# Kernel tuning notes

Hardware: AMD Instinct MI355X
Metric: run time of the kernel (lower is better)

Reference implementation:

```python
import jax, jax.numpy as jnp
import numpy as np

N_QUBITS = 12
DEPTH = 6
BATCH = 4096

# Wire 0 is the most-significant bit (PennyLane default.qubit convention).

def _rx(t):
    c = jnp.cos(t / 2).astype(jnp.complex64)
    s = (-1j * jnp.sin(t / 2)).astype(jnp.complex64)
    return jnp.stack([jnp.stack([c, s], -1), jnp.stack([s, c], -1)], -2)

def _ry(t):
    c = jnp.cos(t / 2).astype(jnp.complex64)
    s = jnp.sin(t / 2).astype(jnp.complex64)
    return jnp.stack([jnp.stack([c, -s], -1), jnp.stack([s, c], -1)], -2)

def _rz(t):
    em = jnp.exp(-1j * t.astype(jnp.complex64) / 2)
    ep = jnp.exp(1j * t.astype(jnp.complex64) / 2)
    z = jnp.zeros_like(em)
    return jnp.stack([jnp.stack([em, z], -1), jnp.stack([z, ep], -1)], -2)

def _apply_1q(state, gate, q, n):
    # state: (B, 2^n); gate: (2,2) shared or (B,2,2) batched
    B = state.shape[0]
    st = state.reshape(B, 1 << q, 2, 1 << (n - 1 - q))
    eq = 'ab,xlbr->xlar' if gate.ndim == 2 else 'xab,xlbr->xlar'
    return jnp.einsum(eq, gate, st).reshape(B, -1)

def _apply_cnot(state, c, n):
    # CNOT with control c, target c+1 (adjacent wires)
    B = state.shape[0]
    st = state.reshape(B, 1 << c, 2, 2, 1 << (n - 2 - c))
    st = jnp.concatenate([st[:, :, 0:1], st[:, :, 1:2, ::-1]], axis=2)
    return st.reshape(B, -1)

def _z_signs(n):
    idx = jnp.arange(1 << n)
    bits = (idx[None, :] >> (n - 1 - jnp.arange(n))[:, None]) & 1  # (n, 2^n)
    return (1.0 - 2.0 * bits).astype(jnp.float32)

def setup_inputs() -> dict:
    key = jax.random.key(0)
    k1, k2 = jax.random.split(key)
    x = jax.random.normal(k1, (BATCH, N_QUBITS), dtype=jnp.float32)
    params = jax.random.normal(k2, (DEPTH, N_QUBITS, 3), dtype=jnp.float32)
    return {"x": x, "params": params}

def reference(x, params):
    B, n = x.shape
    depth = params.shape[0]
    state = jnp.zeros((B, 1 << n), jnp.complex64).at[:, 0].set(1.0)
    # input encoding: batched RX per qubit
    for i in range(n):
        state = _apply_1q(state, _rx(x[:, i]), i, n)
    for d in range(depth):
        for i in range(n):
            state = _apply_1q(state, _ry(params[d, i, 0]), i, n)
            state = _apply_1q(state, _rz(params[d, i, 1]), i, n)
            state = _apply_1q(state, _rx(params[d, i, 2]), i, n)
        for i in range(n - 1):
            state = _apply_cnot(state, i, n)
    probs = state.real ** 2 + state.imag ** 2  # (B, 2^n)
    return probs @ _z_signs(n).T  # (B, n) Pauli-Z expvals
```

## Files before the change

### kernel.cpp

```cpp
#include <hip/hip_runtime.h>

#define NQ    12
#define DEPTH 6
#define BLK   256
#define NT    4


typedef __attribute__((ext_vector_type(8))) short bfrag;
typedef __attribute__((ext_vector_type(4))) float f32x4v;
typedef __attribute__((ext_vector_type(4))) int   i32x4v;

__device__ __forceinline__ int sfx4r(int v) { v ^= v >> 1; v ^= v >> 2; return v & 15; }

__device__ __forceinline__ unsigned rne16(unsigned u) {
  return (u + 0x7FFFu + ((u >> 16) & 1u)) >> 16;
}
__device__ __forceinline__ unsigned packsplit(float x) {
  const unsigned u = __float_as_uint(x);
  const unsigned h = rne16(u);
  const float hf = __uint_as_float(h << 16);
  const unsigned l = rne16(__float_as_uint(x - hf));
  return h | (l << 16);
}

__global__ void prep_kernel(const float* __restrict__ params, float* __restrict__ gt) {
  const int s18 = blockIdx.x;
  const int d = s18 / 3, p = s18 % 3;
  const int L = threadIdx.x;
  __shared__ float G[4][8];
  if (L < 4) {
    const int wire = 11 - 4 * p - L;
    const float py = params[(d * NQ + wire) * 3 + 0];
    const float pz = params[(d * NQ + wire) * 3 + 1];
    const float px = params[(d * NQ + wire) * 3 + 2];
    float sa, ca, sb, cb, sg, cg;
    __sincosf(py * 0.5f, &sa, &ca);
    __sincosf(pz * 0.5f, &sb, &cb);
    __sincosf(px * 0.5f, &sg, &cg);
    const float Ar = ca * cb, Ai = -ca * sb;
    const float Br = -sa * cb, Bi = sa * sb;
    const float Cr = sa * cb, Ci = sa * sb;
    const float Dr = ca * cb, Di = ca * sb;
    float* u = G[L];
    u[0] = cg * Ar + sg * Ci;  u[1] = cg * Ai - sg * Cr;
    u[2] = cg * Br + sg * Di;  u[3] = cg * Bi - sg * Dr;
    u[4] = sg * Ai + cg * Cr;  u[5] = -sg * Ar + cg * Ci;
    u[6] = sg * Bi + cg * Dr;  u[7] = -sg * Br + cg * Di;
  }
  __syncthreads();
  const int r = L & 15, kg = L >> 4;
  unsigned short frag[4][8];
#pragma unroll
  for (int e = 0; e < 8; ++e) {
    const int kk = ((kg & 1) << 3) | e;
    float cr = 1.f, ci = 0.f;
#pragma unroll
    for (int bb = 0; bb < 4; ++bb) {
      const int cell = (((r >> bb) & 1) * 2 + ((kk >> bb) & 1)) * 2;
      const float ar = G[bb][cell], ai = G[bb][cell + 1];
      const float nr = cr * ar - ci * ai;
      const float ni = cr * ai + ci * ar;
      cr = nr; ci = ni;
    }
    const float vr = (kg >= 2) ? -ci : cr;
    const float vi = (kg >= 2) ?  cr : ci;
    const unsigned wr = packsplit(vr);
    const unsigned wi = packsplit(vi);
    frag[0][e] = (unsigned short)(wr & 0xFFFFu);
    frag[1][e] = (unsigned short)(wr >> 16);
    frag[2][e] = (unsigned short)(wi & 0xFFFFu);
    frag[3][e] = (unsigned short)(wi >> 16);
  }
#pragma unroll
  for (int mx = 0; mx < 4; ++mx) {
    const unsigned q0 = (unsigned)frag[mx][0] | ((unsigned)frag[mx][1] << 16);
    const unsigned q1 = (unsigned)frag[mx][2] | ((unsigned)frag[mx][3] << 16);
    const unsigned q2 = (unsigned)frag[mx][4] | ((unsigned)frag[mx][5] << 16);
    const unsigned q3 = (unsigned)frag[mx][6] | ((unsigned)frag[mx][7] << 16);
    i32x4v vv = { (int)q0, (int)q1, (int)q2, (int)q3 };
    *(i32x4v*)((char*)gt + (((s18 * 4 + mx) * 64) + L) * 16) = vv;
  }
}

template <int P, bool FINAL>
__device__ __forceinline__ void do_sweep(int d, const float* __restrict__ gt,
                                         char* smb, int T, float* vout) {
  const int lane = T & 63, wvi = T >> 6;
  const int n = lane & 15, g = lane >> 4;
  const int comp = g >> 1, lhalf = g & 1;
  const int s18 = d * 3 + P;

  const i32x4v* gp = (const i32x4v*)gt + s18 * 4 * 64 + lane;
  const bfrag G0 = __builtin_bit_cast(bfrag, gp[0]);
  const bfrag G1 = __builtin_bit_cast(bfrag, gp[64]);
  const bfrag G2 = __builtin_bit_cast(bfrag, gp[128]);
  const bfrag G3 = __builtin_bit_cast(bfrag, gp[192]);

  f32x4v rlo[NT], rhi[NT];
#pragma unroll
  for (int t = 0; t < NT; ++t) {
    const int TT = 4 * t + wvi;
    const int c = TT * 16 + n;
    const int chunk0 = ((comp * 4 + lhalf * 2) ^ n ^ TT) & 7;
    const int base = c * 128 + chunk0 * 16;
    rlo[t] = *(const f32x4v*)(smb + base);
    rhi[t] = *(const f32x4v*)(smb + (base ^ 16));
  }
  __syncthreads();

  float ts[NT], Dv0[NT], Dv1[NT];
  const int sfxn = sfx4r(n);
  const int pn = __popc(n) & 1;
  const int sfxg = sfx4r(g << 2);

#pragma unroll
  for (int t = 0; t < NT; ++t) {
    const int TT = 4 * t + wvi;
    unsigned SHu[4], SLu[4];
#pragma unroll
    for (int p = 0; p < 4; ++p) {
      const int e = 2 * p;
      const int h = e >> 2;
      const f32x4v rv = h ? rhi[t] : rlo[t];
      const float a  = rv[(e & 3) ^ (t & 3)];
      const float b2 = rv[((e + 1) & 3) ^ (t & 3)];
      const unsigned au = __float_as_uint(a), bu = __float_as_uint(b2);
      const float ha = __uint_as_float(au & 0xFFFF0000u);
      const float hb = __uint_as_float(bu & 0xFFFF0000u);
      const float la = a - ha, lb = b2 - hb;
      SHu[p] = __builtin_amdgcn_perm(bu, au, 0x07060302u);
      unsigned pk;
      asm("v_cvt_pk_bf16_f32 %0, %1, %2" : "=v"(pk) : "v"(la), "v"(lb));
      SLu[p] = pk;
    }
    i32x4v hv = { (int)SHu[0], (int)SHu[1], (int)SHu[2], (int)SHu[3] };
    i32x4v lv = { (int)SLu[0], (int)SLu[1], (int)SLu[2], (int)SLu[3] };
    const bfrag SH = __builtin_bit_cast(bfrag, hv);
    const bfrag SL = __builtin_bit_cast(bfrag, lv);

    f32x4v cr = {0.f, 0.f, 0.f, 0.f}, ci = {0.f, 0.f, 0.f, 0.f};
    cr = __builtin_amdgcn_mfma_f32_16x16x32_bf16(SH, G0, cr, 0, 0, 0);
    cr = __builtin_amdgcn_mfma_f32_16x16x32_bf16(SL, G0, cr, 0, 0, 0);
    cr = __builtin_amdgcn_mfma_f32_16x16x32_bf16(SH, G1, cr, 0, 0, 0);
    ci = __builtin_amdgcn_mfma_f32_16x16x32_bf16(SH, G2, ci, 0, 0, 0);
    ci = __builtin_amdgcn_mfma_f32_16x16x32_bf16(SL, G2, ci, 0, 0, 0);
    ci = __builtin_amdgcn_mfma_f32_16x16x32_bf16(SH, G3, ci, 0, 0, 0);

    if (P == 0) {
      const int c1 = TT * 16 + n;
      const int chR = (g ^ n ^ TT) & 7;
      f32x4v str, sti;
#pragma unroll
      for (int dw = 0; dw < 4; ++dw) { str[dw] = cr[dw ^ (t & 3)]; sti[dw] = ci[dw ^ (t & 3)]; }
      *(f32x4v*)(smb + c1 * 128 + chR * 16) = str;
      *(f32x4v*)(smb + c1 * 128 + (chR ^ 4) * 16) = sti;
    } else if (P == 1) {
#pragma unroll
      for (int dd = 0; dd < 4; ++dd) {
        const int c2 = 16 * n + 4 * g + dd;
        const int chR = (t ^ ((4 * g + dd) ^ n)) & 7;
        const int dw = (wvi ^ (n >> 2)) & 3;
        *(float*)(smb + c2 * 128 + chR * 16 + dw * 4) = cr[dd];
        *(float*)(smb + c2 * 128 + (chR ^ 4) * 16 + dw * 4) = ci[dd];
      }
    } else if (!FINAL) {
      const int sfxT = sfx4r(TT), pT = __popc(TT) & 1;
      const int pmh15 = ((pT ^ pn) ? 15 : 0);
      const int mlow = (sfxT ^ (pn ? 15 : 0)) & 15;
      const int c0 = (sfxn << 4) | mlow;
      const int S3c0 = (mlow ^ sfxn) & 7;
      const int s2c0 = (sfxn >> 2) & 3;
      const int SFXDD[4] = {0, 1, 3, 2};
#pragma unroll
      for (int dd = 0; dd < 4; ++dd) {
        const int l0 = (sfxg ^ SFXDD[dd] ^ pmh15) & 15;
        const int ch = ((l0 >> 2) ^ S3c0) & 7;
        const int dw = ((l0 & 3) ^ s2c0) & 3;
        *(float*)(smb + c0 * 128 + ch * 16 + dw * 4) = cr[dd];
        *(float*)(smb + c0 * 128 + (ch ^ 4) * 16 + dw * 4) = ci[dd];
      }
    } else {
      float pr0 = fmaf(cr[0], cr[0], ci[0] * ci[0]);
      float pr1 = fmaf(cr[1], cr[1], ci[1] * ci[1]);
      float pr2 = fmaf(cr[2], cr[2], ci[2] * ci[2]);
      float pr3 = fmaf(cr[3], cr[3], ci[3] * ci[3]);
      ts[t]  = (pr0 + pr1) + (pr2 + pr3);
      Dv0[t] = (pr0 + pr3) - (pr1 + pr2);
      Dv1[t] = (pr0 + pr1) - (pr2 + pr3);
    }
  }

  if (!FINAL) {
    __syncthreads();
  } else {
    const float sT  = (ts[0] + ts[1]) + (ts[2] + ts[3]);
    const float sB2 = (ts[0] + ts[3]) - (ts[1] + ts[2]);
    const float sB3 = (ts[0] + ts[1]) - (ts[2] + ts[3]);
    const float sD0 = (Dv0[0] + Dv0[3]) - (Dv0[1] + Dv0[2]);
    const float sD1 = (Dv1[0] + Dv1[3]) - (Dv1[1] + Dv1[2]);
    const float pnf   = pn ? -1.f : 1.f;
    const float wvpf  = ((wvi ^ (wvi >> 1)) & 1) ? -1.f : 1.f;
    const float wv1f  = ((wvi >> 1) & 1) ? -1.f : 1.f;
    const float g1f   = ((g >> 1) & 1) ? -1.f : 1.f;
    const float pg01f = ((g ^ (g >> 1)) & 1) ? -1.f : 1.f;
    vout[0] = ((sfxn >> 3) & 1) ? -sT : sT;
    vout[1] = ((sfxn >> 2) & 1) ? -sT : sT;
    vout[2] = ((sfxn >> 1) & 1) ? -sT : sT;
    vout[3] = (sfxn & 1) ? -sT : sT;
    const float pB2 = pnf * sB2;
    vout[4] = pnf * sB3;
    vout[5] = pB2;
    vout[6] = wv1f * pB2;
    vout[7] = wvpf * pB2;
    vout[8] = g1f * wvpf * pB2;
    vout[9] = pg01f * wvpf * pB2;
    vout[10] = pg01f * pnf * wvpf * sD1;
    vout[11] = pg01f * pnf * wvpf * sD0;
  }
}

__global__ __launch_bounds__(BLK) void qsim_kernel(const float* __restrict__ x,
                                                   const float* __restrict__ gt,
                                                   float* __restrict__ out) {
  __shared__ __align__(16) char smb[32768];
  const int T = threadIdx.x, b = blockIdx.x;

  {
    float cs[NQ], sn[NQ];
#pragma unroll
    for (int i = 0; i < NQ; ++i) __sincosf(x[b * NQ + i] * 0.5f, &sn[i], &cs[i]);
    float hm = 1.0f;
#pragma unroll
    for (int i = 0; i < 8; ++i) hm *= ((T >> (7 - i)) & 1) ? sn[i] : cs[i];
    float mag[16];
    mag[0] = hm;
#pragma unroll
    for (int bb = 0; bb < 4; ++bb)
#pragma unroll
      for (int j = 0; j < (1 << bb); ++j) {
        mag[j | (1 << bb)] = mag[j] * sn[11 - bb];
        mag[j]             = mag[j] * cs[11 - bb];
      }
    const int pt = __popc(T);
    const int S3T = (T ^ (T >> 4)) & 7;
    const int s2T = (T >> 6) & 3;
#pragma unroll
    for (int l = 0; l < 16; ++l) {
      const float m = mag[l];
      const int k = (pt + __popc(l)) & 3;
      const float rr = (k & 1) ? 0.f : ((k & 2) ? -m : m);
      const float ii = (k & 1) ? ((k & 2) ? m : -m) : 0.f;
      const int ch = ((l >> 2) ^ S3T) & 7;
      const int dw = ((l & 3) ^ s2T) & 3;
      *(float*)(smb + T * 128 + ch * 16 + dw * 4) = rr;
      *(float*)(smb + T * 128 + (ch ^ 4) * 16 + dw * 4) = ii;
    }
  }
  __syncthreads();

  float v[NQ];
#pragma unroll 1
  for (int d = 0; d < DEPTH - 1; ++d) {
    do_sweep<0, false>(d, gt, smb, T, v);
    do_sweep<1, false>(d, gt, smb, T, v);
    do_sweep<2, false>(d, gt, smb, T, v);
  }
  do_sweep<0, false>(DEPTH - 1, gt, smb, T, v);
  do_sweep<1, false>(DEPTH - 1, gt, smb, T, v);
  do_sweep<2, true >(DEPTH - 1, gt, smb, T, v);

#pragma unroll
  for (int w = 0; w < NQ; ++w)
#pragma unroll
    for (int o = 32; o > 0; o >>= 1) v[w] += __shfl_xor(v[w], o);
  float* scr = (float*)smb;
  const int wvi = T >> 6;
  if ((T & 63) == 0)
#pragma unroll
    for (int w = 0; w < NQ; ++w) scr[w * 4 + wvi] = v[w];
  __syncthreads();
  if (T < NQ) out[b * NQ + T] = (scr[T * 4 + 0] + scr[T * 4 + 1]) +
                                (scr[T * 4 + 2] + scr[T * 4 + 3]);
}

extern "C" void kernel_launch(void* const* d_in, const int* in_sizes, int n_in,
                              void* d_out, int out_size, void* d_ws, size_t ws_size,
                              hipStream_t stream) {
  const float* x      = (const float*)d_in[0];
  const float* params = (const float*)d_in[1];
  float* out          = (float*)d_out;
  float* gt           = (float*)d_ws;
  const int B = in_sizes[0] / NQ;
  prep_kernel<<<18, 64, 0, stream>>>(params, gt);
  qsim_kernel<<<B, BLK, 0, stream>>>(x, gt, out);
}
```

Before: 223.0 us.

## Drop barriers around P0 sweep, raise MFMA priority, precompute LDS store addresses

Removes both __syncthreads in the P==0 sweep, and the post-read barrier in the FINAL sweep, on the premise that each wave writes only the LDS slots it read itself in that pass. A barrier is added before the final reduction scratch write to keep it safe. The MFMA block is wrapped in s_setprio to favour matrix issue, and the per-element LDS store addresses for P1/P2 are rewritten as XOR offsets from one base. It relies on the wave-private LDS footprint claim being correct, and a race would silently corrupt the state.

```diff
diff --git a/kernel.cpp b/kernel.cpp
--- a/kernel.cpp
+++ b/kernel.cpp
@@ -106,7 +106,7 @@
     rlo[t] = *(const f32x4v*)(smb + base);
     rhi[t] = *(const f32x4v*)(smb + (base ^ 16));
   }
-  __syncthreads();
+  if (P != 0 && !FINAL) __syncthreads();
 
   float ts[NT], Dv0[NT], Dv1[NT];
   const int sfxn = sfx4r(n);
@@ -139,12 +139,14 @@
     const bfrag SL = __builtin_bit_cast(bfrag, lv);
 
     f32x4v cr = {0.f, 0.f, 0.f, 0.f}, ci = {0.f, 0.f, 0.f, 0.f};
+    __builtin_amdgcn_s_setprio(1);
     cr = __builtin_amdgcn_mfma_f32_16x16x32_bf16(SH, G0, cr, 0, 0, 0);
     cr = __builtin_amdgcn_mfma_f32_16x16x32_bf16(SL, G0, cr, 0, 0, 0);
     cr = __builtin_amdgcn_mfma_f32_16x16x32_bf16(SH, G1, cr, 0, 0, 0);
     ci = __builtin_amdgcn_mfma_f32_16x16x32_bf16(SH, G2, ci, 0, 0, 0);
     ci = __builtin_amdgcn_mfma_f32_16x16x32_bf16(SL, G2, ci, 0, 0, 0);
     ci = __builtin_amdgcn_mfma_f32_16x16x32_bf16(SH, G3, ci, 0, 0, 0);
+    __builtin_amdgcn_s_setprio(0);
 
     if (P == 0) {
       const int c1 = TT * 16 + n;
@@ -155,14 +157,14 @@
       *(f32x4v*)(smb + c1 * 128 + chR * 16) = str;
       *(f32x4v*)(smb + c1 * 128 + (chR ^ 4) * 16) = sti;
     } else if (P == 1) {
-#pragma unroll
-      for (int dd = 0; dd < 4; ++dd) {
-        const int c2 = 16 * n + 4 * g + dd;
-        const int chR = (t ^ ((4 * g + dd) ^ n)) & 7;
-        const int dw = (wvi ^ (n >> 2)) & 3;
-        *(float*)(smb + c2 * 128 + chR * 16 + dw * 4) = cr[dd];
-        *(float*)(smb + c2 * 128 + (chR ^ 4) * 16 + dw * 4) = ci[dd];
-      }
+      const int c20 = 16 * n + 4 * g;
+      const int chR0 = (t ^ (4 * g) ^ n) & 7;
+      const int dwP1 = (wvi ^ (n >> 2)) & 3;
+      const int A0 = c20 * 128 + chR0 * 16 + dwP1 * 4;
+      *(float*)(smb + (A0        )) = cr[0];  *(float*)(smb + (A0 ^  64)) = ci[0];
+      *(float*)(smb + (A0 ^ 0x090)) = cr[1];  *(float*)(smb + (A0 ^ 0x0D0)) = ci[1];
+      *(float*)(smb + (A0 ^ 0x120)) = cr[2];  *(float*)(smb + (A0 ^ 0x160)) = ci[2];
+      *(float*)(smb + (A0 ^ 0x1B0)) = cr[3];  *(float*)(smb + (A0 ^ 0x1F0)) = ci[3];
     } else if (!FINAL) {
       const int sfxT = sfx4r(TT), pT = __popc(TT) & 1;
       const int pmh15 = ((pT ^ pn) ? 15 : 0);
@@ -170,15 +172,14 @@
       const int c0 = (sfxn << 4) | mlow;
       const int S3c0 = (mlow ^ sfxn) & 7;
       const int s2c0 = (sfxn >> 2) & 3;
-      const int SFXDD[4] = {0, 1, 3, 2};
-#pragma unroll
-      for (int dd = 0; dd < 4; ++dd) {
-        const int l0 = (sfxg ^ SFXDD[dd] ^ pmh15) & 15;
-        const int ch = ((l0 >> 2) ^ S3c0) & 7;
-        const int dw = ((l0 & 3) ^ s2c0) & 3;
-        *(float*)(smb + c0 * 128 + ch * 16 + dw * 4) = cr[dd];
-        *(float*)(smb + c0 * 128 + (ch ^ 4) * 16 + dw * 4) = ci[dd];
-      }
+      const int l00 = (sfxg ^ pmh15) & 15;
+      const int ch0 = ((l00 >> 2) ^ S3c0) & 7;
+      const int dw0 = ((l00 & 3) ^ s2c0) & 3;
+      const int B0 = c0 * 128 + ch0 * 16 + dw0 * 4;
+      *(float*)(smb + (B0     )) = cr[0];  *(float*)(smb + (B0 ^ 64)) = ci[0];
+      *(float*)(smb + (B0 ^  4)) = cr[1];  *(float*)(smb + (B0 ^ 68)) = ci[1];
+      *(float*)(smb + (B0 ^ 12)) = cr[2];  *(float*)(smb + (B0 ^ 76)) = ci[2];
+      *(float*)(smb + (B0 ^  8)) = cr[3];  *(float*)(smb + (B0 ^ 72)) = ci[3];
     } else {
       float pr0 = fmaf(cr[0], cr[0], ci[0] * ci[0]);
       float pr1 = fmaf(cr[1], cr[1], ci[1] * ci[1]);
@@ -190,9 +191,9 @@
     }
   }
 
-  if (!FINAL) {
+  if (P != 0 && !FINAL) {
     __syncthreads();
-  } else {
+  } else if (FINAL) {
     const float sT  = (ts[0] + ts[1]) + (ts[2] + ts[3]);
     const float sB2 = (ts[0] + ts[3]) - (ts[1] + ts[2]);
     const float sB3 = (ts[0] + ts[1]) - (ts[2] + ts[3]);
@@ -273,6 +274,7 @@
   for (int w = 0; w < NQ; ++w)
 #pragma unroll
     for (int o = 32; o > 0; o >>= 1) v[w] += __shfl_xor(v[w], o);
+  __syncthreads();
   float* scr = (float*)smb;
   const int wvi = T >> 6;
   if ((T & 63) == 0)
```

After: 216.1 us. 3.1% less time.
